# Optimization experiments

Hardware: AMD Instinct MI355X
Metric: run time of the kernel (lower is better)

## Reference

```python
import jax, jax.numpy as jnp
import numpy as np

B, T, A, H, E = 512, 64, 32, 512, 32


def sinusoidal_pos_encoding(t, dim):
    # t: (B, T) float positions -> (B, T, dim)
    half = dim // 2
    freqs = jnp.exp(-jnp.log(10000.0) * jnp.arange(half, dtype=jnp.float32) / half)
    ang = t[..., None] * freqs  # (B, T, half)
    return jnp.concatenate([jnp.sin(ang), jnp.cos(ang)], axis=-1)


def cat_linear(x, W, b, cat_ids):
    # x: (B, T, Din); W: (E, Din, Dout); b: (E, Dout); cat_ids: (B,)
    Wg = W[cat_ids]            # (B, Din, Dout) gathered per-sample weights
    bg = b[cat_ids][:, None]   # (B, 1, Dout)
    return jnp.einsum('btd,bdh->bth', x, Wg) + bg


def swish(x):
    return x * jax.nn.sigmoid(x)


def setup_inputs() -> dict:
    key = jax.random.key(0)
    ks = jax.random.split(key, 10)
    s = lambda fan_in: 1.0 / np.sqrt(fan_in)
    return {
        'actions': jax.random.normal(ks[0], (B, T, A), dtype=jnp.float32),
        'timesteps': jax.random.uniform(ks[1], (B,), dtype=jnp.float32),
        'cat_ids': jax.random.randint(ks[2], (B,), 0, E),
        'W1': jax.random.normal(ks[3], (E, A, H), dtype=jnp.float32) * s(A),
        'b1': jnp.zeros((E, H), dtype=jnp.float32),
        'W2': jax.random.normal(ks[4], (E, 2 * H, H), dtype=jnp.float32) * s(2 * H),
        'b2': jnp.zeros((E, H), dtype=jnp.float32),
        'W3': jax.random.normal(ks[5], (E, H, H), dtype=jnp.float32) * s(H),
        'b3': jnp.zeros((E, H), dtype=jnp.float32),
    }


def reference(actions, timesteps, cat_ids, W1, b1, W2, b2, W3, b3):
    b, t, _ = actions.shape
    timesteps_bt = jnp.broadcast_to(timesteps[:, None], (b, t))
    a_emb = cat_linear(actions, W1, b1, cat_ids)              # (B, T, H)
    tau_emb = sinusoidal_pos_encoding(timesteps_bt, H).astype(a_emb.dtype)
    x = jnp.concatenate([a_emb, tau_emb], axis=-1)            # (B, T, 2H)
    x = swish(cat_linear(x, W2, b2, cat_ids))                 # (B, T, H)
    x = cat_linear(x, W3, b3, cat_ids)                        # (B, T, H)
    return x
```

## Files before the change

### kernel.cpp

```cpp
#include <hip/hip_runtime.h>
#include <hip/hip_bf16.h>

#define B_ 512
#define T_ 64
#define A_ 32
#define H_ 512
#define E_ 32
#define MAX_TASKS 272

typedef unsigned short u16;
typedef unsigned int u32;
typedef __attribute__((ext_vector_type(8))) short short8;
typedef __attribute__((ext_vector_type(4))) float floatx4;

static __device__ __forceinline__ u16 f2bf(float f) {
    u32 u = __builtin_bit_cast(u32, f);
    u += 0x7fffu + ((u >> 16) & 1u);
    return (u16)(u >> 16);
}

__global__ void group_kernel(const int* __restrict__ cat_ids,
                             int* __restrict__ sample_list,
                             int4* __restrict__ tasks) {
    __shared__ int cnt[E_], off[E_], cur[E_];
    int tid = threadIdx.x;
    if (tid < E_) { cnt[tid] = 0; cur[tid] = 0; }
    __syncthreads();
    int e = cat_ids[tid];
    atomicAdd(&cnt[e], 1);
    __syncthreads();
    if (tid == 0) {
        int run = 0;
        for (int i = 0; i < E_; i++) { off[i] = run; run += cnt[i]; }
        int ti = 0;
        for (int i = 0; i < E_; i++) {
            int c = cnt[i];
            for (int j = 0; j < c; j += 2)
                tasks[ti++] = make_int4(i, off[i] + j, (c - j >= 2) ? 2 : 1, 0);
        }
        for (; ti < MAX_TASKS; ti++) tasks[ti] = make_int4(0, 0, 0, 0);
    }
    __syncthreads();
    int p = atomicAdd(&cur[e], 1);
    sample_list[off[e] + p] = tid;
}

__global__ __launch_bounds__(256) void embed_kernel(
        const float* __restrict__ actions, const float* __restrict__ timesteps,
        const int* __restrict__ cat_ids, const float* __restrict__ W1,
        const float* __restrict__ b1, u16* __restrict__ a_emb,
        u16* __restrict__ tau_emb) {
    int b = blockIdx.x;
    int tid = threadIdx.x;
    int e = cat_ids[b];
    float tval = timesteps[b];

    {
        float freq = expf(-9.210340371976184f * (float)tid * (1.0f / 256.0f));
        float ang = tval * freq;
        tau_emb[b * H_ + tid]       = f2bf(sinf(ang));
        tau_emb[b * H_ + 256 + tid] = f2bf(cosf(ang));
    }

    __shared__ float act[T_ * A_];
    const float* asrc = actions + (size_t)b * T_ * A_;
    for (int i = tid; i < T_ * A_; i += 256) act[i] = asrc[i];
    __syncthreads();

    const float* w1 = W1 + (size_t)e * A_ * H_;
    int n0 = tid, n1 = tid + 256;
    float wA[A_], wB[A_];
#pragma unroll
    for (int k = 0; k < A_; k++) {
        wA[k] = w1[k * H_ + n0];
        wB[k] = w1[k * H_ + n1];
    }
    float bA = b1[e * H_ + n0], bB = b1[e * H_ + n1];
    u16* orow = a_emb + (size_t)b * T_ * H_;
    for (int tt = 0; tt < T_; tt++) {
        float accA = bA, accB = bB;
#pragma unroll
        for (int k = 0; k < A_; k++) {
            float a = act[tt * A_ + k];
            accA = fmaf(a, wA[k], accA);
            accB = fmaf(a, wB[k], accB);
        }
        orow[tt * H_ + n0] = f2bf(accA);
        orow[tt * H_ + n1] = f2bf(accB);
    }
}

template <int DIN, bool HAS_TAU, bool DO_SWISH, bool OUT_BF16>
__global__ __launch_bounds__(256, 2) void moe_gemm(
        const u16* __restrict__ xsrc, const u16* __restrict__ tau,
        const float* __restrict__ W, const float* __restrict__ bias,
        const int* __restrict__ sample_list, const int4* __restrict__ tasks,
        void* __restrict__ outp) {
    int4 task = tasks[blockIdx.y];
    int ns = task.z;
    if (ns == 0) return;
    int e = task.x;
    int s0 = sample_list[task.y];
    int s1 = (ns > 1) ? sample_list[task.y + 1] : s0;
    int n0 = blockIdx.x * 128;

    int tid = threadIdx.x;
    int lane = tid & 63, wv = tid >> 6, quad = lane >> 4, c15 = lane & 15;

    __shared__ __align__(16) u16 xs[128 * 40];
    __shared__ __align__(16) u16 wt[128 * 40];

    floatx4 acc[2][8];
    floatx4 zero4 = {0.f, 0.f, 0.f, 0.f};
#pragma unroll
    for (int i = 0; i < 2; i++)
#pragma unroll
        for (int j = 0; j < 8; j++) acc[i][j] = zero4;

    const float* wbase = W + (size_t)e * DIN * H_ + n0;
    int x_row = tid >> 2, x_oct = tid & 3;
    int w_nn = tid & 127, w_kh = tid >> 7;

    for (int k0 = 0; k0 < DIN; k0 += 32) {
        bool use_tau = HAS_TAU && (k0 >= 512);
#pragma unroll
        for (int h = 0; h < 2; h++) {
            int row = x_row + h * 64;
            int s = (row < 64) ? s0 : s1;
            int t = row & 63;
            int kg = k0 + x_oct * 8;
            const u16* src = use_tau ? (tau + (size_t)s * H_ + (kg - 512))
                                     : (xsrc + ((size_t)s * T_ + t) * H_ + kg);
            short8 v = *(const short8*)src;
            *(short8*)&xs[row * 40 + x_oct * 8] = v;
        }
        {
            const float* wp = wbase + (size_t)(k0 + w_kh * 16) * H_ + w_nn;
            short8 h0, h1;
#pragma unroll
            for (int j = 0; j < 8; j++) {
                h0[j] = (short)f2bf(wp[(size_t)j * H_]);
                h1[j] = (short)f2bf(wp[(size_t)(j + 8) * H_]);
            }
            *(short8*)&wt[w_nn * 40 + w_kh * 16]     = h0;
            *(short8*)&wt[w_nn * 40 + w_kh * 16 + 8] = h1;
        }
        __syncthreads();

        short8 af[2], bf[8];
#pragma unroll
        for (int mt = 0; mt < 2; mt++) {
            int row = wv * 32 + mt * 16 + c15;
            af[mt] = *(const short8*)&xs[row * 40 + quad * 8];
        }
#pragma unroll
        for (int nt = 0; nt < 8; nt++) {
            int nr = nt * 16 + c15;
            bf[nt] = *(const short8*)&wt[nr * 40 + quad * 8];
        }
#pragma unroll
        for (int mt = 0; mt < 2; mt++)
#pragma unroll
            for (int nt = 0; nt < 8; nt++)
                acc[mt][nt] = __builtin_amdgcn_mfma_f32_16x16x32_bf16(
                        af[mt], bf[nt], acc[mt][nt], 0, 0, 0);
        __syncthreads();
    }

    const float* bp = bias + (size_t)e * H_;
#pragma unroll
    for (int mt = 0; mt < 2; mt++) {
        int rbase = wv * 32 + mt * 16 + quad * 4;
        int side = rbase >> 6;
        if (side == 1 && ns == 1) continue;
        int s = side ? s1 : s0;
#pragma unroll
        for (int nt = 0; nt < 8; nt++) {
            int col = n0 + nt * 16 + c15;
            float bv = bp[col];
#pragma unroll
            for (int r = 0; r < 4; r++) {
                int t = (rbase + r) & 63;
                float v = acc[mt][nt][r] + bv;
                if (DO_SWISH) v = v / (1.0f + expf(-v));
                size_t oidx = ((size_t)s * T_ + t) * H_ + col;
                if (OUT_BF16) ((u16*)outp)[oidx] = f2bf(v);
                else          ((float*)outp)[oidx] = v;
            }
        }
    }
}

extern "C" void kernel_launch(void* const* d_in, const int* in_sizes, int n_in,
                              void* d_out, int out_size, void* d_ws, size_t ws_size,
                              hipStream_t stream) {
    const float* actions   = (const float*)d_in[0];
    const float* timesteps = (const float*)d_in[1];
    const int*   cat_ids   = (const int*)d_in[2];
    const float* W1 = (const float*)d_in[3];
    const float* b1 = (const float*)d_in[4];
    const float* W2 = (const float*)d_in[5];
    const float* b2 = (const float*)d_in[6];
    const float* W3 = (const float*)d_in[7];
    const float* b3 = (const float*)d_in[8];

    char* ws = (char*)d_ws;
    u16* a_emb = (u16*)ws;
    u16* y     = (u16*)(ws + (size_t)32 * 1024 * 1024);
    u16* tau   = (u16*)(ws + (size_t)64 * 1024 * 1024);
    int* sample_list = (int*)(ws + (size_t)64 * 1024 * 1024 + 512 * 1024);
    int4* tasks = (int4*)(ws + (size_t)64 * 1024 * 1024 + 512 * 1024 + 4096);

    hipLaunchKernelGGL(group_kernel, dim3(1), dim3(512), 0, stream,
                       cat_ids, sample_list, tasks);
    hipLaunchKernelGGL(embed_kernel, dim3(512), dim3(256), 0, stream,
                       actions, timesteps, cat_ids, W1, b1, a_emb, tau);
    hipLaunchKernelGGL((moe_gemm<2 * H_, true, true, true>), dim3(4, MAX_TASKS),
                       dim3(256), 0, stream,
                       a_emb, tau, W2, b2, sample_list, tasks, (void*)y);
    hipLaunchKernelGGL((moe_gemm<H_, false, false, false>), dim3(4, MAX_TASKS),
                       dim3(256), 0, stream,
                       y, (const u16*)nullptr, W3, b3, sample_list, tasks, d_out);
}
```

Measured before the change: 320.3 us.

## Pre-convert expert weights to transposed bf16 and retile MoE GEMM as 2x2 warps

Adds a convert_transpose kernel that turns W2 and W3 into bf16 laid out [E][N][K] once per call, so the GEMM loads weight tiles as contiguous 16-byte vectors instead of strided fp32 loads converted inside the k-loop. The GEMM now steps K by 64, uses a 2x2 wave layout with 4x4 MFMA tiles per wave, and raises launch bounds to 3 blocks per SM. The group kernel also writes the task list in parallel across experts. The transposed weights are stored in d_out and a_emb buffers that are reused as scratch, which adds two extra kernels and a full weight pass but amortizes conversion across the ~8 tasks that share each expert.

```diff
diff --git a/kernel.cpp b/kernel.cpp
--- a/kernel.cpp
+++ b/kernel.cpp
@@ -22,7 +22,8 @@
 __global__ void group_kernel(const int* __restrict__ cat_ids,
                              int* __restrict__ sample_list,
                              int4* __restrict__ tasks) {
-    __shared__ int cnt[E_], off[E_], cur[E_];
+    __shared__ int cnt[E_], off[E_], cur[E_], toff[E_];
+    __shared__ int total;
     int tid = threadIdx.x;
     if (tid < E_) { cnt[tid] = 0; cur[tid] = 0; }
     __syncthreads();
@@ -30,17 +31,21 @@
     atomicAdd(&cnt[e], 1);
     __syncthreads();
     if (tid == 0) {
-        int run = 0;
-        for (int i = 0; i < E_; i++) { off[i] = run; run += cnt[i]; }
-        int ti = 0;
+        int run = 0, trun = 0;
         for (int i = 0; i < E_; i++) {
-            int c = cnt[i];
-            for (int j = 0; j < c; j += 2)
-                tasks[ti++] = make_int4(i, off[i] + j, (c - j >= 2) ? 2 : 1, 0);
-        }
-        for (; ti < MAX_TASKS; ti++) tasks[ti] = make_int4(0, 0, 0, 0);
-    }
-    __syncthreads();
+            off[i] = run;  run += cnt[i];
+            toff[i] = trun; trun += (cnt[i] + 1) >> 1;
+        }
+        total = trun;
+    }
+    __syncthreads();
+    if (tid < E_) {
+        int c = cnt[tid], o = off[tid], to = toff[tid];
+        for (int j = 0; j < c; j += 2)
+            tasks[to++] = make_int4(tid, o + j, (c - j >= 2) ? 2 : 1, 0);
+    }
+    for (int i = total + tid; i < MAX_TASKS; i += 512)
+        tasks[i] = make_int4(0, 0, 0, 0);
     int p = atomicAdd(&cur[e], 1);
     sample_list[off[e] + p] = tid;
 }
@@ -90,10 +95,27 @@
     }
 }
 
+__global__ __launch_bounds__(256) void convert_transpose(
+        const float* __restrict__ W, u16* __restrict__ Wt, int K) {
+    int n = blockIdx.y * 256 + threadIdx.x;
+    int k0 = blockIdx.x * 32;
+    int e = blockIdx.z;
+    const float* src = W + ((size_t)e * K + k0) * H_ + n;
+    short8 out[4];
+#pragma unroll
+    for (int j = 0; j < 32; j++)
+        out[j >> 3][j & 7] = (short)f2bf(src[(size_t)j * H_]);
+    u16* dst = Wt + ((size_t)e * H_ + n) * K + k0;
+#pragma unroll
+    for (int c = 0; c < 4; c++) *(short8*)(dst + c * 8) = out[c];
+}
+
+#define LDSTR 72
+
 template <int DIN, bool HAS_TAU, bool DO_SWISH, bool OUT_BF16>
-__global__ __launch_bounds__(256, 2) void moe_gemm(
+__global__ __launch_bounds__(256, 3) void moe_gemm(
         const u16* __restrict__ xsrc, const u16* __restrict__ tau,
-        const float* __restrict__ W, const float* __restrict__ bias,
+        const u16* __restrict__ Wt, const float* __restrict__ bias,
         const int* __restrict__ sample_list, const int4* __restrict__ tasks,
         void* __restrict__ outp) {
     int4 task = tasks[blockIdx.y];
@@ -105,78 +127,74 @@
     int n0 = blockIdx.x * 128;
 
     int tid = threadIdx.x;
-    int lane = tid & 63, wv = tid >> 6, quad = lane >> 4, c15 = lane & 15;
-
-    __shared__ __align__(16) u16 xs[128 * 40];
-    __shared__ __align__(16) u16 wt[128 * 40];
-
-    floatx4 acc[2][8];
+    int lane = tid & 63, wv = tid >> 6;
+    int wr = wv >> 1, wc = wv & 1;
+    int quad = lane >> 4, c15 = lane & 15;
+
+    __shared__ __align__(16) u16 xs[128 * LDSTR];
+    __shared__ __align__(16) u16 wt[128 * LDSTR];
+
+    floatx4 acc[4][4];
     floatx4 zero4 = {0.f, 0.f, 0.f, 0.f};
 #pragma unroll
-    for (int i = 0; i < 2; i++)
-#pragma unroll
-        for (int j = 0; j < 8; j++) acc[i][j] = zero4;
-
-    const float* wbase = W + (size_t)e * DIN * H_ + n0;
-    int x_row = tid >> 2, x_oct = tid & 3;
-    int w_nn = tid & 127, w_kh = tid >> 7;
-
-    for (int k0 = 0; k0 < DIN; k0 += 32) {
+    for (int i = 0; i < 4; i++)
+#pragma unroll
+        for (int j = 0; j < 4; j++) acc[i][j] = zero4;
+
+    const u16* wbase = Wt + (size_t)(e * H_ + n0) * DIN;
+    int sr = tid >> 2;
+    int sk = (tid & 3) * 16;
+
+    for (int k0 = 0; k0 < DIN; k0 += 64) {
         bool use_tau = HAS_TAU && (k0 >= 512);
 #pragma unroll
         for (int h = 0; h < 2; h++) {
-            int row = x_row + h * 64;
+            int row = sr + h * 64;
             int s = (row < 64) ? s0 : s1;
             int t = row & 63;
-            int kg = k0 + x_oct * 8;
-            const u16* src = use_tau ? (tau + (size_t)s * H_ + (kg - 512))
-                                     : (xsrc + ((size_t)s * T_ + t) * H_ + kg);
-            short8 v = *(const short8*)src;
-            *(short8*)&xs[row * 40 + x_oct * 8] = v;
-        }
-        {
-            const float* wp = wbase + (size_t)(k0 + w_kh * 16) * H_ + w_nn;
-            short8 h0, h1;
-#pragma unroll
-            for (int j = 0; j < 8; j++) {
-                h0[j] = (short)f2bf(wp[(size_t)j * H_]);
-                h1[j] = (short)f2bf(wp[(size_t)(j + 8) * H_]);
+            const u16* src = use_tau
+                ? (tau + (size_t)s * H_ + (k0 - 512) + sk)
+                : (xsrc + ((size_t)s * T_ + t) * H_ + k0 + sk);
+            *(short8*)&xs[row * LDSTR + sk]     = *(const short8*)src;
+            *(short8*)&xs[row * LDSTR + sk + 8] = *(const short8*)(src + 8);
+        }
+#pragma unroll
+        for (int h = 0; h < 2; h++) {
+            int nn = sr + h * 64;
+            const u16* src = wbase + (size_t)nn * DIN + k0 + sk;
+            *(short8*)&wt[nn * LDSTR + sk]     = *(const short8*)src;
+            *(short8*)&wt[nn * LDSTR + sk + 8] = *(const short8*)(src + 8);
+        }
+        __syncthreads();
+
+#pragma unroll
+        for (int kk = 0; kk < 2; kk++) {
+            short8 af[4], bfr[4];
+#pragma unroll
+            for (int i = 0; i < 4; i++) {
+                af[i]  = *(const short8*)&xs[(wr * 64 + i * 16 + c15) * LDSTR + kk * 32 + quad * 8];
+                bfr[i] = *(const short8*)&wt[(wc * 64 + i * 16 + c15) * LDSTR + kk * 32 + quad * 8];
             }
-            *(short8*)&wt[w_nn * 40 + w_kh * 16]     = h0;
-            *(short8*)&wt[w_nn * 40 + w_kh * 16 + 8] = h1;
+#pragma unroll
+            for (int mt = 0; mt < 4; mt++)
+#pragma unroll
+                for (int nt = 0; nt < 4; nt++)
+                    acc[mt][nt] = __builtin_amdgcn_mfma_f32_16x16x32_bf16(
+                            af[mt], bfr[nt], acc[mt][nt], 0, 0, 0);
         }
         __syncthreads();
-
-        short8 af[2], bf[8];
-#pragma unroll
-        for (int mt = 0; mt < 2; mt++) {
-            int row = wv * 32 + mt * 16 + c15;
-            af[mt] = *(const short8*)&xs[row * 40 + quad * 8];
-        }
-#pragma unroll
-        for (int nt = 0; nt < 8; nt++) {
-            int nr = nt * 16 + c15;
-            bf[nt] = *(const short8*)&wt[nr * 40 + quad * 8];
-        }
-#pragma unroll
-        for (int mt = 0; mt < 2; mt++)
-#pragma unroll
-            for (int nt = 0; nt < 8; nt++)
-                acc[mt][nt] = __builtin_amdgcn_mfma_f32_16x16x32_bf16(
-                        af[mt], bf[nt], acc[mt][nt], 0, 0, 0);
-        __syncthreads();
     }
 
     const float* bp = bias + (size_t)e * H_;
 #pragma unroll
-    for (int mt = 0; mt < 2; mt++) {
-        int rbase = wv * 32 + mt * 16 + quad * 4;
+    for (int mt = 0; mt < 4; mt++) {
+        int rbase = wr * 64 + mt * 16 + quad * 4;
         int side = rbase >> 6;
         if (side == 1 && ns == 1) continue;
         int s = side ? s1 : s0;
 #pragma unroll
-        for (int nt = 0; nt < 8; nt++) {
-            int col = n0 + nt * 16 + c15;
+        for (int nt = 0; nt < 4; nt++) {
+            int col = n0 + wc * 64 + nt * 16 + c15;
             float bv = bp[col];
 #pragma unroll
             for (int r = 0; r < 4; r++) {
@@ -210,15 +228,21 @@
     u16* tau   = (u16*)(ws + (size_t)64 * 1024 * 1024);
     int* sample_list = (int*)(ws + (size_t)64 * 1024 * 1024 + 512 * 1024);
     int4* tasks = (int4*)(ws + (size_t)64 * 1024 * 1024 + 512 * 1024 + 4096);
+    u16* Wt2 = (u16*)d_out;
+    u16* Wt3 = a_emb;
 
     hipLaunchKernelGGL(group_kernel, dim3(1), dim3(512), 0, stream,
                        cat_ids, sample_list, tasks);
     hipLaunchKernelGGL(embed_kernel, dim3(512), dim3(256), 0, stream,
                        actions, timesteps, cat_ids, W1, b1, a_emb, tau);
+    hipLaunchKernelGGL(convert_transpose, dim3(2 * H_ / 32, 2, E_), dim3(256),
+                       0, stream, W2, Wt2, 2 * H_);
     hipLaunchKernelGGL((moe_gemm<2 * H_, true, true, true>), dim3(4, MAX_TASKS),
                        dim3(256), 0, stream,
-                       a_emb, tau, W2, b2, sample_list, tasks, (void*)y);
+                       a_emb, tau, Wt2, b2, sample_list, tasks, (void*)y);
+    hipLaunchKernelGGL(convert_transpose, dim3(H_ / 32, 2, E_), dim3(256),
+                       0, stream, W3, Wt3, H_);
     hipLaunchKernelGGL((moe_gemm<H_, false, false, false>), dim3(4, MAX_TASKS),
                        dim3(256), 0, stream,
-                       y, (const u16*)nullptr, W3, b3, sample_list, tasks, d_out);
-}
+                       y, (const u16*)nullptr, Wt3, b3, sample_list, tasks, d_out);
+}
```

Result: slower. 351.8 us (+9.9%).
